# Kernel tuning notes

Measured on AMD Instinct MI355X. Metric: run time of the kernel, lower is better.

The kernel has to match this reference:

```python
import jax, jax.numpy as jnp
import numpy as np


def setup_inputs() -> dict:
    key = jax.random.key(0)
    ks = jax.random.split(key, 10)
    B, L, H, E, D = 2, 2048, 16, 64, 64
    d_model = 512
    inp = {
        "queries": jax.random.normal(ks[0], (B, L, H, E), jnp.float32),
        "keys": jax.random.normal(ks[1], (B, L, H, E), jnp.float32),
        "values": jax.random.normal(ks[2], (B, L, H, D), jnp.float32),
        "raw_series": jax.random.normal(ks[3], (B, L, d_model), jnp.float32),
        # learned fusion MLP: Linear(d_model, d_model//2) -> ReLU -> Linear(d_model//2, 1)
        "w1": jax.random.normal(ks[4], (d_model, d_model // 2), jnp.float32) / np.sqrt(d_model),
        "b1": jnp.zeros((d_model // 2,), jnp.float32),
        "w2": jax.random.normal(ks[5], (d_model // 2, 1), jnp.float32) / np.sqrt(d_model // 2),
        "b2": jnp.zeros((1,), jnp.float32),
        # per-head trend scaling, init ones
        "alpha_trend": jnp.ones((H,), jnp.float32),
    }
    return inp


MOMENTUM_ALPHA = 1.0
MOMENTUM_K = 1


def reference(queries, keys, values, raw_series, w1, b1, w2, b2, alpha_trend):
    B, L, H, E = queries.shape
    scale = 1.0 / jnp.sqrt(jnp.asarray(E, queries.dtype))

    # ---- soft momentum bias ----
    # learned fusion: MLP over features -> scalar per position, [B, L]
    h = jax.nn.relu(raw_series @ w1 + b1)
    fused = (h @ w2 + b2)[..., 0]                       # [B, L]
    k = max(1, min(MOMENTUM_K, L - 1))
    momentum = fused[:, k:] - fused[:, :-k]              # [B, L-k]
    momentum = jnp.pad(momentum, ((0, 0), (k, 0)))       # left-pad zeros -> [B, L]
    diff = jnp.abs(momentum[:, :, None] - momentum[:, None, :])  # [B, L, L]
    soft_bias = -MOMENTUM_ALPHA * diff                   # [B, L, L]

    # ---- attention ----
    scores = jnp.einsum('blhe,bshe->bhls', queries, keys)  # [B, H, L, L]
    scores = scores + soft_bias[:, None, :, :] * alpha_trend[None, :, None, None]
    causal = jnp.triu(jnp.ones((L, L), bool), k=1)       # True above diagonal
    scores = jnp.where(causal[None, None], -jnp.inf, scores)
    A = jax.nn.softmax(scale * scores, axis=-1)          # [B, H, L, L]
    V = jnp.einsum('bhls,bshd->blhd', A, values)         # [B, L, H, D]
    return V
```

## Files before the change

### kernel.cpp

```cpp
#include <hip/hip_runtime.h>
#include <math.h>

#define B_ 2
#define L_ 2048
#define H_ 16
#define E_ 64
#define D_ 64
#define DM_ 512
#define DH_ 256

typedef __bf16 bf16_t;
typedef bf16_t bf16x8_t __attribute__((ext_vector_type(8)));
typedef float f32x4_t __attribute__((ext_vector_type(4)));

__device__ __forceinline__ unsigned bpack(float hi, float lo) {
    unsigned uh = __float_as_uint(hi) + 0x8000u;
    unsigned ul = __float_as_uint(lo) + 0x8000u;
    return __builtin_amdgcn_perm(uh, ul, 0x07060302u);
}

__device__ __forceinline__ bf16_t to_bf16(float f) {
    union { float f; unsigned u; } x; x.f = f;
    unsigned r = (x.u + 0x7fffu + ((x.u >> 16) & 1u)) >> 16;
    union { unsigned short s; bf16_t b; } y; y.s = (unsigned short)r;
    return y.b;
}

__device__ __forceinline__ void gload_lds16(const bf16_t* g, bf16_t* l) {
    __builtin_amdgcn_global_load_lds(
        (const __attribute__((address_space(1))) unsigned int*)g,
        (__attribute__((address_space(3))) unsigned int*)l, 16, 0, 0);
}

__device__ __forceinline__ int permK(int sl) {
    return (sl & 3) | (((sl >> 3) & 1) << 2) | (((sl >> 4) & 1) << 3)
         | (((sl >> 2) & 1) << 4) | (((sl >> 5) & 1) << 5);
}

__global__ __launch_bounds__(256) void prep_kernel(
        const float* __restrict__ w1, bf16_t* __restrict__ w1t,
        const float* __restrict__ K, bf16_t* __restrict__ Kp,
        const float* __restrict__ V, bf16_t* __restrict__ Vs) {
    __shared__ bf16_t T[64][88];
    const int bidx = blockIdx.x;
    const int t = threadIdx.x;

    if (bidx < 256) {
        const int n = bidx;
        #pragma unroll
        for (int u = 0; u < 2; ++u) {
            int k = t + u * 256;
            w1t[(size_t)n * DM_ + k] = to_bf16(w1[(size_t)k * DH_ + n]);
        }
        return;
    }

    if (bidx < 1280) {
        const int idx = bidx - 256;
        const int bh = idx >> 5, tile = idx & 31;
        const int b = bh >> 4, h = bh & 15;
        const int sl = t >> 2, e0 = (t & 3) << 4;
        const float* src = K + (((size_t)b * L_ + tile * 64 + sl) * H_ + h) * E_ + e0;
        f32x4_t v0 = *(const f32x4_t*)(src);
        f32x4_t v1 = *(const f32x4_t*)(src + 4);
        f32x4_t v2 = *(const f32x4_t*)(src + 8);
        f32x4_t v3 = *(const f32x4_t*)(src + 12);
        uint4 lo, hi;
        lo.x = bpack(v0[1], v0[0]); lo.y = bpack(v0[3], v0[2]);
        lo.z = bpack(v1[1], v1[0]); lo.w = bpack(v1[3], v1[2]);
        hi.x = bpack(v2[1], v2[0]); hi.y = bpack(v2[3], v2[2]);
        hi.z = bpack(v3[1], v3[0]); hi.w = bpack(v3[3], v3[2]);
        const int r = permK(sl);
        const int bb = r & 7;
        bf16_t* drow = Kp + ((size_t)(bh * 32 + tile) * 64 + r) * 64;
        *(uint4*)(drow + ((((e0 >> 3)    ) ^ bb) << 3)) = lo;
        *(uint4*)(drow + ((((e0 >> 3) + 1) ^ bb) << 3)) = hi;
        return;
    }

    {
        const int idx = bidx - 1280;
        const int bh = idx >> 5, tile = idx & 31;
        const int b = bh >> 4, h = bh & 15;
        const int sl = t >> 2, d0 = (t & 3) << 4;
        const float* src = V + (((size_t)b * L_ + tile * 64 + sl) * H_ + h) * D_ + d0;
        f32x4_t v0 = *(const f32x4_t*)(src);
        f32x4_t v1 = *(const f32x4_t*)(src + 4);
        f32x4_t v2 = *(const f32x4_t*)(src + 8);
        f32x4_t v3 = *(const f32x4_t*)(src + 12);
        uint4 lo, hi;
        lo.x = bpack(v0[1], v0[0]); lo.y = bpack(v0[3], v0[2]);
        lo.z = bpack(v1[1], v1[0]); lo.w = bpack(v1[3], v1[2]);
        hi.x = bpack(v2[1], v2[0]); hi.y = bpack(v2[3], v2[2]);
        hi.z = bpack(v3[1], v3[0]); hi.w = bpack(v3[3], v3[2]);
        *(uint4*)&T[sl][d0]     = lo;
        *(uint4*)&T[sl][d0 + 8] = hi;
        __syncthreads();
        const int d = t & 63, bd = d & 7;
        bf16_t* drow = Vs + ((size_t)bh * 64 + d) * 2048 + tile * 64;
        #pragma unroll
        for (int gg = 0; gg < 2; ++gg) {
            int qb = (t >> 6) + gg * 4;
            int slb = (qb ^ bd) << 3;
            union { unsigned short u[8]; uint4 q; } acc;
            #pragma unroll
            for (int j = 0; j < 8; ++j) {
                union { bf16_t b; unsigned short s; } x; x.b = T[slb + j][d];
                acc.u[j] = x.s;
            }
            *(uint4*)(drow + qb * 8) = acc.q;
        }
    }
}

__global__ __launch_bounds__(256) void mlp_kernel(
        const float* __restrict__ raw, const bf16_t* __restrict__ w1t,
        const float* __restrict__ b1, const float* __restrict__ w2,
        const float* __restrict__ b2, float* __restrict__ fused) {
    __shared__ bf16_t Rs[16][520];
    __shared__ float part[4][16];
    const int t = threadIdx.x;
    const int m0 = blockIdx.x * 16;
    #pragma unroll
    for (int u = 0; u < 8; ++u) {
        int idx = t + u * 256;
        int row = idx >> 7;
        int k = (idx & 127) << 2;
        f32x4_t v = *(const f32x4_t*)&raw[(size_t)(m0 + row) * DM_ + k];
        uint2 p;
        p.x = bpack(v[1], v[0]);
        p.y = bpack(v[3], v[2]);
        *(uint2*)&Rs[row][k] = p;
    }
    __syncthreads();
    const int wave = t >> 6;
    const int lane = t & 63;
    const int lrow = lane & 15;
    const int lgrp = lane >> 4;
    const int n0w = wave * 64;

    f32x4_t acc[4];
    #pragma unroll
    for (int nt = 0; nt < 4; ++nt) acc[nt] = (f32x4_t){0.f, 0.f, 0.f, 0.f};

    const bf16_t* wbase = w1t + (size_t)(n0w + lrow) * DM_ + lgrp * 8;
    #pragma unroll
    for (int s = 0; s < 16; ++s) {
        bf16x8_t a = *(const bf16x8_t*)&Rs[lrow][s * 32 + lgrp * 8];
        #pragma unroll
        for (int nt = 0; nt < 4; ++nt) {
            bf16x8_t b = *(const bf16x8_t*)(wbase + nt * 16 * DM_ + s * 32);
            acc[nt] = __builtin_amdgcn_mfma_f32_16x16x32_bf16(a, b, acc[nt], 0, 0, 0);
        }
    }
    float rowpart[4] = {0.f, 0.f, 0.f, 0.f};
    #pragma unroll
    for (int nt = 0; nt < 4; ++nt) {
        int n = n0w + nt * 16 + lrow;
        float b1v = b1[n];
        float w2v = w2[n];
        #pragma unroll
        for (int r = 0; r < 4; ++r) {
            float h = acc[nt][r] + b1v;
            h = h > 0.f ? h : 0.f;
            rowpart[r] += h * w2v;
        }
    }
    #pragma unroll
    for (int r = 0; r < 4; ++r) {
        float v = rowpart[r];
        v += __shfl_xor(v, 1);
        v += __shfl_xor(v, 2);
        v += __shfl_xor(v, 4);
        v += __shfl_xor(v, 8);
        if (lrow == 0) part[wave][lgrp * 4 + r] = v;
    }
    __syncthreads();
    if (t < 16)
        fused[m0 + t] = part[0][t] + part[1][t] + part[2][t] + part[3][t] + b2[0];
}

__global__ __launch_bounds__(256) void attn_kernel(
        const float* __restrict__ Q, const bf16_t* __restrict__ Kp,
        const bf16_t* __restrict__ Vs, const float* __restrict__ fused,
        const float* __restrict__ alpha_trend, float* __restrict__ out) {
    __shared__ __align__(16) bf16_t Ks[2][64][64];
    __shared__ __align__(16) bf16_t Vt[2][64][64];
    __shared__ float moms[2][64];

    const int bid = blockIdx.x;
    const int bh  = bid & 31;
    const int grp = bid >> 5;
    const int qt  = (grp & 1) ? (grp >> 1) : 31 - (grp >> 1);
    const int h = bh & 15, b = bh >> 4;
    const int q0 = qt << 6;
    const int tid = threadIdx.x;
    const int wave = tid >> 6, lane = tid & 63;
    const int lrow = lane & 15, lgrp = lane >> 4;

    const float c1 = 0.18033688f;
    const float ascale2 = alpha_trend[h] * c1;
    const size_t bl = (size_t)b * L_;
    const int qw0 = q0 + wave * 16;

    const bf16_t* Kb = Kp + (size_t)bh * 131072;
    const bf16_t* Vb = Vs + (size_t)bh * 131072;
    const float* fusedp = fused + bl;

    bf16x8_t a_lo, a_hi;
    {
        const float* qp = Q + ((bl + qw0 + lrow) * H_ + h) * E_ + lgrp * 8;
        f32x4_t v0 = *(const f32x4_t*)(qp);
        f32x4_t v1 = *(const f32x4_t*)(qp + 4);
        f32x4_t v2 = *(const f32x4_t*)(qp + 32);
        f32x4_t v3 = *(const f32x4_t*)(qp + 36);
        #pragma unroll
        for (int k = 0; k < 4; ++k) {
            a_lo[k]     = to_bf16(v0[k] * c1);
            a_lo[4 + k] = to_bf16(v1[k] * c1);
            a_hi[k]     = to_bf16(v2[k] * c1);
            a_hi[4 + k] = to_bf16(v3[k] * c1);
        }
    }
    const int qg = qw0 + lrow;
    const float mq = (qg == 0) ? 0.f : fusedp[qg] - fusedp[qg - 1];

    const bf16_t* ksrc = Kb + wave * 512 + lane * 8;
    const bf16_t* vsrc = Vb + (size_t)(wave * 8 + (lane >> 3)) * 2048 + (lane & 7) * 8;

    f32x4_t Oacc[4];
    #pragma unroll
    for (int c = 0; c < 4; ++c) Oacc[c] = (f32x4_t){0.f, 0.f, 0.f, 0.f};
    float rowsum = 0.f;

    auto stage = [&](int t) {
        const int nb = t & 1;
        const bf16_t* kp0 = ksrc + (size_t)t * 4096;
        gload_lds16(kp0,        &Ks[nb][wave * 8][0]);
        gload_lds16(kp0 + 2048, &Ks[nb][wave * 8 + 32][0]);
        const bf16_t* vp0 = vsrc + t * 64;
        gload_lds16(vp0,               &Vt[nb][wave * 8][0]);
        gload_lds16(vp0 + 32 * 2048,   &Vt[nb][wave * 8 + 32][0]);
        if (tid < 64) {
            int s = t * 64 + tid;
            float f = fusedp[s];
            float fm = __shfl_up(f, 1);
            if (tid == 0) fm = (s == 0) ? f : fusedp[s - 1];
            moms[nb][tid] = f - fm;
        }
    };

    stage(0);
    for (int st = 0; st <= qt; ++st) {
        const int buf = st & 1;
        __syncthreads();
        if (st < qt) stage(st + 1);

        const char* ksb = (const char*)&Ks[buf][0][0];
        const char* vtb = (const char*)&Vt[buf][0][0];
        const int bb = lrow & 7;

        f32x4_t Sacc[4];
        #pragma unroll
        for (int c = 0; c < 4; ++c) Sacc[c] = (f32x4_t){0.f, 0.f, 0.f, 0.f};
        __builtin_amdgcn_s_setprio(1);
        #pragma unroll
        for (int c = 0; c < 4; ++c) {
            const char* kr = ksb + (c * 16 + lrow) * 128;
            bf16x8_t k_lo = *(const bf16x8_t*)(kr + ((lgrp ^ bb) << 4));
            bf16x8_t k_hi = *(const bf16x8_t*)(kr + (((4 + lgrp) ^ bb) << 4));
            Sacc[c] = __builtin_amdgcn_mfma_f32_16x16x32_bf16(k_lo, a_lo, Sacc[c], 0, 0, 0);
            Sacc[c] = __builtin_amdgcn_mfma_f32_16x16x32_bf16(k_hi, a_hi, Sacc[c], 0, 0, 0);
        }
        __builtin_amdgcn_s_setprio(0);

        float rowe[4][4];
        #pragma unroll
        for (int c = 0; c < 4; ++c) {
            const int sb = lgrp * 8 + ((c & 1) << 2) + ((c >> 1) << 5);
            f32x4_t ms4 = *(const f32x4_t*)&moms[buf][sb];
            #pragma unroll
            for (int r = 0; r < 4; ++r) {
                float arg = Sacc[c][r] - ascale2 * fabsf(mq - ms4[r]);
                rowe[c][r] = __builtin_amdgcn_exp2f(arg);
            }
        }
        if (st == qt) {
            const int s0 = st << 6;
            #pragma unroll
            for (int c = 0; c < 4; ++c) {
                const int sg0 = s0 + lgrp * 8 + ((c & 1) << 2) + ((c >> 1) << 5);
                #pragma unroll
                for (int r = 0; r < 4; ++r)
                    if (sg0 + r > qg) rowe[c][r] = 0.f;
            }
        }
        #pragma unroll
        for (int c = 0; c < 4; ++c)
            rowsum += (rowe[c][0] + rowe[c][1]) + (rowe[c][2] + rowe[c][3]);

        #pragma unroll
        for (int hh = 0; hh < 2; ++hh) {
            union { unsigned u[4]; bf16x8_t v; } pa;
            pa.u[0] = bpack(rowe[2 * hh][1],     rowe[2 * hh][0]);
            pa.u[1] = bpack(rowe[2 * hh][3],     rowe[2 * hh][2]);
            pa.u[2] = bpack(rowe[2 * hh + 1][1], rowe[2 * hh + 1][0]);
            pa.u[3] = bpack(rowe[2 * hh + 1][3], rowe[2 * hh + 1][2]);
            __builtin_amdgcn_s_setprio(1);
            #pragma unroll
            for (int c2 = 0; c2 < 4; ++c2) {
                const int row = c2 * 16 + lrow;
                bf16x8_t bv = *(const bf16x8_t*)(vtb + row * 128 +
                                                 (((hh * 4 + lgrp) ^ bb) << 4));
                Oacc[c2] = __builtin_amdgcn_mfma_f32_16x16x32_bf16(pa.v, bv, Oacc[c2], 0, 0, 0);
            }
            __builtin_amdgcn_s_setprio(0);
        }
    }

    float rs = rowsum;
    rs += __shfl_xor(rs, 16);
    rs += __shfl_xor(rs, 32);
    #pragma unroll
    for (int r = 0; r < 4; ++r) {
        float inv = 1.f / __shfl(rs, lgrp * 4 + r);
        size_t orow = ((bl + qw0 + lgrp * 4 + r) * H_ + h) * D_;
        #pragma unroll
        for (int c = 0; c < 4; ++c)
            out[orow + c * 16 + lrow] = Oacc[c][r] * inv;
    }
}

extern "C" void kernel_launch(void* const* d_in, const int* in_sizes, int n_in,
                              void* d_out, int out_size, void* d_ws, size_t ws_size,
                              hipStream_t stream) {
    const float* Q     = (const float*)d_in[0];
    const float* K     = (const float*)d_in[1];
    const float* V     = (const float*)d_in[2];
    const float* raw   = (const float*)d_in[3];
    const float* w1    = (const float*)d_in[4];
    const float* b1    = (const float*)d_in[5];
    const float* w2    = (const float*)d_in[6];
    const float* b2    = (const float*)d_in[7];
    const float* alpha = (const float*)d_in[8];
    float* out = (float*)d_out;

    float* fused = (float*)d_ws;
    bf16_t* w1t  = (bf16_t*)(fused + B_ * L_);
    bf16_t* Kp   = w1t + 256 * 512;
    bf16_t* Vs   = Kp + (size_t)B_ * H_ * L_ * E_;

    prep_kernel<<<2304, 256, 0, stream>>>(w1, w1t, K, Kp, V, Vs);
    mlp_kernel<<<B_ * L_ / 16, 256, 0, stream>>>(raw, w1t, b1, w2, b2, fused);
    attn_kernel<<<B_ * H_ * (L_ / 64), 256, 0, stream>>>(Q, Kp, Vs, fused, alpha, out);
}
```

Measured before the change: 169.5 us.

## Widen attention query tile to 128 rows and split MLP across N with atomics

The attention kernel now processes 128 query rows per block, with each wave handling two 16-row sub-tiles. Each staged K/V tile is reused for twice the queries, which halves K/V loads per query. Waves whose rows lie entirely before a key tile skip its compute, and blocks pair light and heavy tiles for causal balance. The MLP kernel is split four ways over hidden units, with partial sums combined by atomicAdd into a zeroed fused buffer and b2 dropped because momentum is a difference. The costs are more register pressure, half as many attention blocks, and idle waves on diagonal tiles.

```diff
diff --git a/kernel.cpp b/kernel.cpp
--- a/kernel.cpp
+++ b/kernel.cpp
@@ -40,7 +40,8 @@
 __global__ __launch_bounds__(256) void prep_kernel(
         const float* __restrict__ w1, bf16_t* __restrict__ w1t,
         const float* __restrict__ K, bf16_t* __restrict__ Kp,
-        const float* __restrict__ V, bf16_t* __restrict__ Vs) {
+        const float* __restrict__ V, bf16_t* __restrict__ Vs,
+        float* __restrict__ fused) {
     __shared__ bf16_t T[64][88];
     const int bidx = blockIdx.x;
     const int t = threadIdx.x;
@@ -51,6 +52,10 @@
         for (int u = 0; u < 2; ++u) {
             int k = t + u * 256;
             w1t[(size_t)n * DM_ + k] = to_bf16(w1[(size_t)k * DH_ + n]);
+        }
+        if (bidx == 0) {
+            #pragma unroll
+            for (int u = 0; u < 16; ++u) fused[t + u * 256] = 0.f;
         }
         return;
     }
@@ -116,11 +121,12 @@
 __global__ __launch_bounds__(256) void mlp_kernel(
         const float* __restrict__ raw, const bf16_t* __restrict__ w1t,
         const float* __restrict__ b1, const float* __restrict__ w2,
-        const float* __restrict__ b2, float* __restrict__ fused) {
+        float* __restrict__ fused) {
     __shared__ bf16_t Rs[16][520];
     __shared__ float part[4][16];
     const int t = threadIdx.x;
-    const int m0 = blockIdx.x * 16;
+    const int m0 = (blockIdx.x >> 2) * 16;
+    const int nq = blockIdx.x & 3;
     #pragma unroll
     for (int u = 0; u < 8; ++u) {
         int idx = t + u * 256;
@@ -137,34 +143,24 @@
     const int lane = t & 63;
     const int lrow = lane & 15;
     const int lgrp = lane >> 4;
-    const int n0w = wave * 64;
-
-    f32x4_t acc[4];
-    #pragma unroll
-    for (int nt = 0; nt < 4; ++nt) acc[nt] = (f32x4_t){0.f, 0.f, 0.f, 0.f};
-
-    const bf16_t* wbase = w1t + (size_t)(n0w + lrow) * DM_ + lgrp * 8;
+    const int n = nq * 64 + wave * 16 + lrow;
+
+    f32x4_t acc = (f32x4_t){0.f, 0.f, 0.f, 0.f};
+    const bf16_t* wbase = w1t + (size_t)n * DM_ + lgrp * 8;
     #pragma unroll
     for (int s = 0; s < 16; ++s) {
         bf16x8_t a = *(const bf16x8_t*)&Rs[lrow][s * 32 + lgrp * 8];
-        #pragma unroll
-        for (int nt = 0; nt < 4; ++nt) {
-            bf16x8_t b = *(const bf16x8_t*)(wbase + nt * 16 * DM_ + s * 32);
-            acc[nt] = __builtin_amdgcn_mfma_f32_16x16x32_bf16(a, b, acc[nt], 0, 0, 0);
-        }
-    }
-    float rowpart[4] = {0.f, 0.f, 0.f, 0.f};
-    #pragma unroll
-    for (int nt = 0; nt < 4; ++nt) {
-        int n = n0w + nt * 16 + lrow;
-        float b1v = b1[n];
-        float w2v = w2[n];
-        #pragma unroll
-        for (int r = 0; r < 4; ++r) {
-            float h = acc[nt][r] + b1v;
-            h = h > 0.f ? h : 0.f;
-            rowpart[r] += h * w2v;
-        }
+        bf16x8_t b = *(const bf16x8_t*)(wbase + s * 32);
+        acc = __builtin_amdgcn_mfma_f32_16x16x32_bf16(a, b, acc, 0, 0, 0);
+    }
+    const float b1v = b1[n];
+    const float w2v = w2[n];
+    float rowpart[4];
+    #pragma unroll
+    for (int r = 0; r < 4; ++r) {
+        float h = acc[r] + b1v;
+        h = h > 0.f ? h : 0.f;
+        rowpart[r] = h * w2v;
     }
     #pragma unroll
     for (int r = 0; r < 4; ++r) {
@@ -177,7 +173,7 @@
     }
     __syncthreads();
     if (t < 16)
-        fused[m0 + t] = part[0][t] + part[1][t] + part[2][t] + part[3][t] + b2[0];
+        atomicAdd(&fused[m0 + t], part[0][t] + part[1][t] + part[2][t] + part[3][t]);
 }
 
 __global__ __launch_bounds__(256) void attn_kernel(
@@ -191,9 +187,10 @@
     const int bid = blockIdx.x;
     const int bh  = bid & 31;
     const int grp = bid >> 5;
-    const int qt  = (grp & 1) ? (grp >> 1) : 31 - (grp >> 1);
+    const int tq  = (grp < 8) ? grp : 23 - grp;
     const int h = bh & 15, b = bh >> 4;
-    const int q0 = qt << 6;
+    const int q0 = tq << 7;
+    const int nsteps = 2 * tq + 2;
     const int tid = threadIdx.x;
     const int wave = tid >> 6, lane = tid & 63;
     const int lrow = lane & 15, lgrp = lane >> 4;
@@ -201,37 +198,51 @@
     const float c1 = 0.18033688f;
     const float ascale2 = alpha_trend[h] * c1;
     const size_t bl = (size_t)b * L_;
-    const int qw0 = q0 + wave * 16;
+    const int qw0 = q0 + wave * 32;
 
     const bf16_t* Kb = Kp + (size_t)bh * 131072;
     const bf16_t* Vb = Vs + (size_t)bh * 131072;
     const float* fusedp = fused + bl;
 
-    bf16x8_t a_lo, a_hi;
+    bf16x8_t a_lo, a_hi, c_lo, c_hi;
     {
         const float* qp = Q + ((bl + qw0 + lrow) * H_ + h) * E_ + lgrp * 8;
         f32x4_t v0 = *(const f32x4_t*)(qp);
         f32x4_t v1 = *(const f32x4_t*)(qp + 4);
         f32x4_t v2 = *(const f32x4_t*)(qp + 32);
         f32x4_t v3 = *(const f32x4_t*)(qp + 36);
+        const float* qp2 = qp + 16 * H_ * E_;
+        f32x4_t w0 = *(const f32x4_t*)(qp2);
+        f32x4_t w1v = *(const f32x4_t*)(qp2 + 4);
+        f32x4_t w2v = *(const f32x4_t*)(qp2 + 32);
+        f32x4_t w3 = *(const f32x4_t*)(qp2 + 36);
         #pragma unroll
         for (int k = 0; k < 4; ++k) {
             a_lo[k]     = to_bf16(v0[k] * c1);
             a_lo[4 + k] = to_bf16(v1[k] * c1);
             a_hi[k]     = to_bf16(v2[k] * c1);
             a_hi[4 + k] = to_bf16(v3[k] * c1);
-        }
-    }
-    const int qg = qw0 + lrow;
-    const float mq = (qg == 0) ? 0.f : fusedp[qg] - fusedp[qg - 1];
+            c_lo[k]     = to_bf16(w0[k] * c1);
+            c_lo[4 + k] = to_bf16(w1v[k] * c1);
+            c_hi[k]     = to_bf16(w2v[k] * c1);
+            c_hi[4 + k] = to_bf16(w3[k] * c1);
+        }
+    }
+    const int qg  = qw0 + lrow;
+    const int qg2 = qg + 16;
+    const float mq  = (qg == 0) ? 0.f : fusedp[qg] - fusedp[qg - 1];
+    const float mq2 = fusedp[qg2] - fusedp[qg2 - 1];
 
     const bf16_t* ksrc = Kb + wave * 512 + lane * 8;
     const bf16_t* vsrc = Vb + (size_t)(wave * 8 + (lane >> 3)) * 2048 + (lane & 7) * 8;
 
-    f32x4_t Oacc[4];
-    #pragma unroll
-    for (int c = 0; c < 4; ++c) Oacc[c] = (f32x4_t){0.f, 0.f, 0.f, 0.f};
-    float rowsum = 0.f;
+    f32x4_t Oacc[4], Oacc2[4];
+    #pragma unroll
+    for (int c = 0; c < 4; ++c) {
+        Oacc[c]  = (f32x4_t){0.f, 0.f, 0.f, 0.f};
+        Oacc2[c] = (f32x4_t){0.f, 0.f, 0.f, 0.f};
+    }
+    float rowsum = 0.f, rowsum2 = 0.f;
 
     auto stage = [&](int t) {
         const int nb = t & 1;
@@ -251,83 +262,105 @@
     };
 
     stage(0);
-    for (int st = 0; st <= qt; ++st) {
+    for (int st = 0; st < nsteps; ++st) {
         const int buf = st & 1;
         __syncthreads();
-        if (st < qt) stage(st + 1);
+        if (st + 1 < nsteps) stage(st + 1);
+
+        const int s0 = st << 6;
+        if (s0 > qw0) continue;
 
         const char* ksb = (const char*)&Ks[buf][0][0];
         const char* vtb = (const char*)&Vt[buf][0][0];
         const int bb = lrow & 7;
 
-        f32x4_t Sacc[4];
-        #pragma unroll
-        for (int c = 0; c < 4; ++c) Sacc[c] = (f32x4_t){0.f, 0.f, 0.f, 0.f};
+        f32x4_t Sacc[4], Sacc2[4];
+        #pragma unroll
+        for (int c = 0; c < 4; ++c) {
+            Sacc[c]  = (f32x4_t){0.f, 0.f, 0.f, 0.f};
+            Sacc2[c] = (f32x4_t){0.f, 0.f, 0.f, 0.f};
+        }
         __builtin_amdgcn_s_setprio(1);
         #pragma unroll
         for (int c = 0; c < 4; ++c) {
             const char* kr = ksb + (c * 16 + lrow) * 128;
             bf16x8_t k_lo = *(const bf16x8_t*)(kr + ((lgrp ^ bb) << 4));
             bf16x8_t k_hi = *(const bf16x8_t*)(kr + (((4 + lgrp) ^ bb) << 4));
-            Sacc[c] = __builtin_amdgcn_mfma_f32_16x16x32_bf16(k_lo, a_lo, Sacc[c], 0, 0, 0);
-            Sacc[c] = __builtin_amdgcn_mfma_f32_16x16x32_bf16(k_hi, a_hi, Sacc[c], 0, 0, 0);
+            Sacc[c]  = __builtin_amdgcn_mfma_f32_16x16x32_bf16(k_lo, a_lo, Sacc[c], 0, 0, 0);
+            Sacc2[c] = __builtin_amdgcn_mfma_f32_16x16x32_bf16(k_lo, c_lo, Sacc2[c], 0, 0, 0);
+            Sacc[c]  = __builtin_amdgcn_mfma_f32_16x16x32_bf16(k_hi, a_hi, Sacc[c], 0, 0, 0);
+            Sacc2[c] = __builtin_amdgcn_mfma_f32_16x16x32_bf16(k_hi, c_hi, Sacc2[c], 0, 0, 0);
         }
         __builtin_amdgcn_s_setprio(0);
 
-        float rowe[4][4];
+        float rowe[4][4], rowe2[4][4];
         #pragma unroll
         for (int c = 0; c < 4; ++c) {
             const int sb = lgrp * 8 + ((c & 1) << 2) + ((c >> 1) << 5);
             f32x4_t ms4 = *(const f32x4_t*)&moms[buf][sb];
             #pragma unroll
             for (int r = 0; r < 4; ++r) {
-                float arg = Sacc[c][r] - ascale2 * fabsf(mq - ms4[r]);
-                rowe[c][r] = __builtin_amdgcn_exp2f(arg);
+                float arg  = Sacc[c][r]  - ascale2 * fabsf(mq  - ms4[r]);
+                float arg2 = Sacc2[c][r] - ascale2 * fabsf(mq2 - ms4[r]);
+                rowe[c][r]  = __builtin_amdgcn_exp2f(arg);
+                rowe2[c][r] = __builtin_amdgcn_exp2f(arg2);
             }
         }
-        if (st == qt) {
-            const int s0 = st << 6;
+        if (qw0 - s0 < 64) {
             #pragma unroll
             for (int c = 0; c < 4; ++c) {
                 const int sg0 = s0 + lgrp * 8 + ((c & 1) << 2) + ((c >> 1) << 5);
                 #pragma unroll
-                for (int r = 0; r < 4; ++r)
-                    if (sg0 + r > qg) rowe[c][r] = 0.f;
+                for (int r = 0; r < 4; ++r) {
+                    if (sg0 + r > qg)  rowe[c][r]  = 0.f;
+                    if (sg0 + r > qg2) rowe2[c][r] = 0.f;
+                }
             }
         }
         #pragma unroll
-        for (int c = 0; c < 4; ++c)
-            rowsum += (rowe[c][0] + rowe[c][1]) + (rowe[c][2] + rowe[c][3]);
+        for (int c = 0; c < 4; ++c) {
+            rowsum  += (rowe[c][0]  + rowe[c][1])  + (rowe[c][2]  + rowe[c][3]);
+            rowsum2 += (rowe2[c][0] + rowe2[c][1]) + (rowe2[c][2] + rowe2[c][3]);
+        }
 
         #pragma unroll
         for (int hh = 0; hh < 2; ++hh) {
-            union { unsigned u[4]; bf16x8_t v; } pa;
-            pa.u[0] = bpack(rowe[2 * hh][1],     rowe[2 * hh][0]);
-            pa.u[1] = bpack(rowe[2 * hh][3],     rowe[2 * hh][2]);
-            pa.u[2] = bpack(rowe[2 * hh + 1][1], rowe[2 * hh + 1][0]);
-            pa.u[3] = bpack(rowe[2 * hh + 1][3], rowe[2 * hh + 1][2]);
+            union { unsigned u[4]; bf16x8_t v; } pa, pa2;
+            pa.u[0]  = bpack(rowe[2 * hh][1],      rowe[2 * hh][0]);
+            pa.u[1]  = bpack(rowe[2 * hh][3],      rowe[2 * hh][2]);
+            pa.u[2]  = bpack(rowe[2 * hh + 1][1],  rowe[2 * hh + 1][0]);
+            pa.u[3]  = bpack(rowe[2 * hh + 1][3],  rowe[2 * hh + 1][2]);
+            pa2.u[0] = bpack(rowe2[2 * hh][1],     rowe2[2 * hh][0]);
+            pa2.u[1] = bpack(rowe2[2 * hh][3],     rowe2[2 * hh][2]);
+            pa2.u[2] = bpack(rowe2[2 * hh + 1][1], rowe2[2 * hh + 1][0]);
+            pa2.u[3] = bpack(rowe2[2 * hh + 1][3], rowe2[2 * hh + 1][2]);
             __builtin_amdgcn_s_setprio(1);
             #pragma unroll
             for (int c2 = 0; c2 < 4; ++c2) {
                 const int row = c2 * 16 + lrow;
                 bf16x8_t bv = *(const bf16x8_t*)(vtb + row * 128 +
                                                  (((hh * 4 + lgrp) ^ bb) << 4));
-                Oacc[c2] = __builtin_amdgcn_mfma_f32_16x16x32_bf16(pa.v, bv, Oacc[c2], 0, 0, 0);
+                Oacc[c2]  = __builtin_amdgcn_mfma_f32_16x16x32_bf16(pa.v,  bv, Oacc[c2],  0, 0, 0);
+                Oacc2[c2] = __builtin_amdgcn_mfma_f32_16x16x32_bf16(pa2.v, bv, Oacc2[c2], 0, 0, 0);
             }
             __builtin_amdgcn_s_setprio(0);
         }
     }
 
-    float rs = rowsum;
-    rs += __shfl_xor(rs, 16);
-    rs += __shfl_xor(rs, 32);
+    float rs = rowsum, rs2 = rowsum2;
+    rs  += __shfl_xor(rs, 16);  rs  += __shfl_xor(rs, 32);
+    rs2 += __shfl_xor(rs2, 16); rs2 += __shfl_xor(rs2, 32);
     #pragma unroll
     for (int r = 0; r < 4; ++r) {
-        float inv = 1.f / __shfl(rs, lgrp * 4 + r);
-        size_t orow = ((bl + qw0 + lgrp * 4 + r) * H_ + h) * D_;
-        #pragma unroll
-        for (int c = 0; c < 4; ++c)
-            out[orow + c * 16 + lrow] = Oacc[c][r] * inv;
+        float inv  = 1.f / __shfl(rs,  lgrp * 4 + r);
+        float inv2 = 1.f / __shfl(rs2, lgrp * 4 + r);
+        size_t orow  = ((bl + qw0 + lgrp * 4 + r) * H_ + h) * D_;
+        size_t orow2 = orow + (size_t)16 * H_ * D_;
+        #pragma unroll
+        for (int c = 0; c < 4; ++c) {
+            out[orow  + c * 16 + lrow] = Oacc[c][r]  * inv;
+            out[orow2 + c * 16 + lrow] = Oacc2[c][r] * inv2;
+        }
     }
 }
 
@@ -341,7 +374,6 @@
     const float* w1    = (const float*)d_in[4];
     const float* b1    = (const float*)d_in[5];
     const float* w2    = (const float*)d_in[6];
-    const float* b2    = (const float*)d_in[7];
     const float* alpha = (const float*)d_in[8];
     float* out = (float*)d_out;
 
@@ -350,7 +382,7 @@
     bf16_t* Kp   = w1t + 256 * 512;
     bf16_t* Vs   = Kp + (size_t)B_ * H_ * L_ * E_;
 
-    prep_kernel<<<2304, 256, 0, stream>>>(w1, w1t, K, Kp, V, Vs);
-    mlp_kernel<<<B_ * L_ / 16, 256, 0, stream>>>(raw, w1t, b1, w2, b2, fused);
-    attn_kernel<<<B_ * H_ * (L_ / 64), 256, 0, stream>>>(Q, Kp, Vs, fused, alpha, out);
-}
+    prep_kernel<<<2304, 256, 0, stream>>>(w1, w1t, K, Kp, V, Vs, fused);
+    mlp_kernel<<<B_ * L_ / 16 * 4, 256, 0, stream>>>(raw, w1t, b1, w2, fused);
+    attn_kernel<<<B_ * H_ * (L_ / 128), 256, 0, stream>>>(Q, Kp, Vs, fused, alpha, out);
+}
```

Result: slower. 179.8 us (+6.1%).

## Process KV tiles in pairs, precompute momentum, split MLP hidden across blocks

Applied to the files above, without the earlier changes.

The attention kernel now stages two 64-key tiles per barrier, so there are half as many __syncthreads per query block. Each block also precomputes momentum for the whole sequence into shared memory once, instead of computing it per tile. The MLP kernel splits the hidden dimension across four blocks per row group and reduces with atomicAdd into a buffer zeroed in prep, which gives it more parallelism. The cost is more LDS per attention block, which may lower occupancy. Dropping b2 is valid because it cancels in the momentum difference, but atomics make the fused sum order non-deterministic.

```diff
diff --git a/kernel.cpp b/kernel.cpp
--- a/kernel.cpp
+++ b/kernel.cpp
@@ -40,7 +40,8 @@
 __global__ __launch_bounds__(256) void prep_kernel(
         const float* __restrict__ w1, bf16_t* __restrict__ w1t,
         const float* __restrict__ K, bf16_t* __restrict__ Kp,
-        const float* __restrict__ V, bf16_t* __restrict__ Vs) {
+        const float* __restrict__ V, bf16_t* __restrict__ Vs,
+        float* __restrict__ fused) {
     __shared__ bf16_t T[64][88];
     const int bidx = blockIdx.x;
     const int t = threadIdx.x;
@@ -51,6 +52,10 @@
         for (int u = 0; u < 2; ++u) {
             int k = t + u * 256;
             w1t[(size_t)n * DM_ + k] = to_bf16(w1[(size_t)k * DH_ + n]);
+        }
+        if (bidx == 0) {
+            #pragma unroll
+            for (int u = 0; u < 16; ++u) fused[t + u * 256] = 0.f;
         }
         return;
     }
@@ -116,11 +121,12 @@
 __global__ __launch_bounds__(256) void mlp_kernel(
         const float* __restrict__ raw, const bf16_t* __restrict__ w1t,
         const float* __restrict__ b1, const float* __restrict__ w2,
-        const float* __restrict__ b2, float* __restrict__ fused) {
+        float* __restrict__ fused) {
     __shared__ bf16_t Rs[16][520];
     __shared__ float part[4][16];
     const int t = threadIdx.x;
-    const int m0 = blockIdx.x * 16;
+    const int m0 = (blockIdx.x >> 2) * 16;
+    const int nq = blockIdx.x & 3;
     #pragma unroll
     for (int u = 0; u < 8; ++u) {
         int idx = t + u * 256;
@@ -137,34 +143,24 @@
     const int lane = t & 63;
     const int lrow = lane & 15;
     const int lgrp = lane >> 4;
-    const int n0w = wave * 64;
-
-    f32x4_t acc[4];
-    #pragma unroll
-    for (int nt = 0; nt < 4; ++nt) acc[nt] = (f32x4_t){0.f, 0.f, 0.f, 0.f};
-
-    const bf16_t* wbase = w1t + (size_t)(n0w + lrow) * DM_ + lgrp * 8;
+    const int n = nq * 64 + wave * 16 + lrow;
+
+    f32x4_t acc = (f32x4_t){0.f, 0.f, 0.f, 0.f};
+    const bf16_t* wbase = w1t + (size_t)n * DM_ + lgrp * 8;
     #pragma unroll
     for (int s = 0; s < 16; ++s) {
         bf16x8_t a = *(const bf16x8_t*)&Rs[lrow][s * 32 + lgrp * 8];
-        #pragma unroll
-        for (int nt = 0; nt < 4; ++nt) {
-            bf16x8_t b = *(const bf16x8_t*)(wbase + nt * 16 * DM_ + s * 32);
-            acc[nt] = __builtin_amdgcn_mfma_f32_16x16x32_bf16(a, b, acc[nt], 0, 0, 0);
-        }
-    }
-    float rowpart[4] = {0.f, 0.f, 0.f, 0.f};
-    #pragma unroll
-    for (int nt = 0; nt < 4; ++nt) {
-        int n = n0w + nt * 16 + lrow;
-        float b1v = b1[n];
-        float w2v = w2[n];
-        #pragma unroll
-        for (int r = 0; r < 4; ++r) {
-            float h = acc[nt][r] + b1v;
-            h = h > 0.f ? h : 0.f;
-            rowpart[r] += h * w2v;
-        }
+        bf16x8_t b = *(const bf16x8_t*)(wbase + s * 32);
+        acc = __builtin_amdgcn_mfma_f32_16x16x32_bf16(a, b, acc, 0, 0, 0);
+    }
+    const float b1v = b1[n];
+    const float w2v = w2[n];
+    float rowpart[4];
+    #pragma unroll
+    for (int r = 0; r < 4; ++r) {
+        float h = acc[r] + b1v;
+        h = h > 0.f ? h : 0.f;
+        rowpart[r] = h * w2v;
     }
     #pragma unroll
     for (int r = 0; r < 4; ++r) {
@@ -177,16 +173,16 @@
     }
     __syncthreads();
     if (t < 16)
-        fused[m0 + t] = part[0][t] + part[1][t] + part[2][t] + part[3][t] + b2[0];
+        atomicAdd(&fused[m0 + t], part[0][t] + part[1][t] + part[2][t] + part[3][t]);
 }
 
 __global__ __launch_bounds__(256) void attn_kernel(
         const float* __restrict__ Q, const bf16_t* __restrict__ Kp,
         const bf16_t* __restrict__ Vs, const float* __restrict__ fused,
         const float* __restrict__ alpha_trend, float* __restrict__ out) {
-    __shared__ __align__(16) bf16_t Ks[2][64][64];
-    __shared__ __align__(16) bf16_t Vt[2][64][64];
-    __shared__ float moms[2][64];
+    __shared__ __align__(16) bf16_t Ks[2][128][64];
+    __shared__ __align__(16) bf16_t Vt[2][128][64];
+    __shared__ __align__(16) float moms_all[2048];
 
     const int bid = blockIdx.x;
     const int bh  = bid & 31;
@@ -194,6 +190,7 @@
     const int qt  = (grp & 1) ? (grp >> 1) : 31 - (grp >> 1);
     const int h = bh & 15, b = bh >> 4;
     const int q0 = qt << 6;
+    const int npairs = (qt + 2) >> 1;
     const int tid = threadIdx.x;
     const int wave = tid >> 6, lane = tid & 63;
     const int lrow = lane & 15, lgrp = lane >> 4;
@@ -206,6 +203,14 @@
     const bf16_t* Kb = Kp + (size_t)bh * 131072;
     const bf16_t* Vb = Vs + (size_t)bh * 131072;
     const float* fusedp = fused + bl;
+
+    #pragma unroll
+    for (int u = 0; u < 8; ++u) {
+        int i = tid + u * 256;
+        float f = fusedp[i];
+        float fm = (i == 0) ? f : fusedp[i - 1];
+        moms_all[i] = f - fm;
+    }
 
     bf16x8_t a_lo, a_hi;
     {
@@ -233,88 +238,91 @@
     for (int c = 0; c < 4; ++c) Oacc[c] = (f32x4_t){0.f, 0.f, 0.f, 0.f};
     float rowsum = 0.f;
 
-    auto stage = [&](int t) {
-        const int nb = t & 1;
-        const bf16_t* kp0 = ksrc + (size_t)t * 4096;
+    auto stage = [&](int p) {
+        const int nb = p & 1;
+        const bf16_t* kp0 = ksrc + (size_t)p * 8192;
         gload_lds16(kp0,        &Ks[nb][wave * 8][0]);
         gload_lds16(kp0 + 2048, &Ks[nb][wave * 8 + 32][0]);
-        const bf16_t* vp0 = vsrc + t * 64;
-        gload_lds16(vp0,               &Vt[nb][wave * 8][0]);
-        gload_lds16(vp0 + 32 * 2048,   &Vt[nb][wave * 8 + 32][0]);
-        if (tid < 64) {
-            int s = t * 64 + tid;
-            float f = fusedp[s];
-            float fm = __shfl_up(f, 1);
-            if (tid == 0) fm = (s == 0) ? f : fusedp[s - 1];
-            moms[nb][tid] = f - fm;
-        }
+        gload_lds16(kp0 + 4096, &Ks[nb][64 + wave * 8][0]);
+        gload_lds16(kp0 + 6144, &Ks[nb][64 + wave * 8 + 32][0]);
+        const bf16_t* vp0 = vsrc + p * 128;
+        gload_lds16(vp0,                  &Vt[nb][wave * 8][0]);
+        gload_lds16(vp0 + 32 * 2048,      &Vt[nb][wave * 8 + 32][0]);
+        gload_lds16(vp0 + 64,             &Vt[nb][64 + wave * 8][0]);
+        gload_lds16(vp0 + 64 + 32 * 2048, &Vt[nb][64 + wave * 8 + 32][0]);
     };
 
     stage(0);
-    for (int st = 0; st <= qt; ++st) {
-        const int buf = st & 1;
+    for (int p = 0; p < npairs; ++p) {
         __syncthreads();
-        if (st < qt) stage(st + 1);
-
-        const char* ksb = (const char*)&Ks[buf][0][0];
-        const char* vtb = (const char*)&Vt[buf][0][0];
+        if (p + 1 < npairs) stage(p + 1);
+        const int nb = p & 1;
         const int bb = lrow & 7;
 
-        f32x4_t Sacc[4];
-        #pragma unroll
-        for (int c = 0; c < 4; ++c) Sacc[c] = (f32x4_t){0.f, 0.f, 0.f, 0.f};
-        __builtin_amdgcn_s_setprio(1);
-        #pragma unroll
-        for (int c = 0; c < 4; ++c) {
-            const char* kr = ksb + (c * 16 + lrow) * 128;
-            bf16x8_t k_lo = *(const bf16x8_t*)(kr + ((lgrp ^ bb) << 4));
-            bf16x8_t k_hi = *(const bf16x8_t*)(kr + (((4 + lgrp) ^ bb) << 4));
-            Sacc[c] = __builtin_amdgcn_mfma_f32_16x16x32_bf16(k_lo, a_lo, Sacc[c], 0, 0, 0);
-            Sacc[c] = __builtin_amdgcn_mfma_f32_16x16x32_bf16(k_hi, a_hi, Sacc[c], 0, 0, 0);
-        }
-        __builtin_amdgcn_s_setprio(0);
-
-        float rowe[4][4];
-        #pragma unroll
-        for (int c = 0; c < 4; ++c) {
-            const int sb = lgrp * 8 + ((c & 1) << 2) + ((c >> 1) << 5);
-            f32x4_t ms4 = *(const f32x4_t*)&moms[buf][sb];
-            #pragma unroll
-            for (int r = 0; r < 4; ++r) {
-                float arg = Sacc[c][r] - ascale2 * fabsf(mq - ms4[r]);
-                rowe[c][r] = __builtin_amdgcn_exp2f(arg);
-            }
-        }
-        if (st == qt) {
-            const int s0 = st << 6;
+        #pragma unroll
+        for (int sub = 0; sub < 2; ++sub) {
+            const int tile = 2 * p + sub;
+            const int s0 = tile << 6;
+            if (s0 > qw0) continue;
+
+            const char* ksb = (const char*)&Ks[nb][sub * 64][0];
+            const char* vtb = (const char*)&Vt[nb][sub * 64][0];
+
+            f32x4_t Sacc[4];
+            #pragma unroll
+            for (int c = 0; c < 4; ++c) Sacc[c] = (f32x4_t){0.f, 0.f, 0.f, 0.f};
+            __builtin_amdgcn_s_setprio(1);
             #pragma unroll
             for (int c = 0; c < 4; ++c) {
-                const int sg0 = s0 + lgrp * 8 + ((c & 1) << 2) + ((c >> 1) << 5);
+                const char* kr = ksb + (c * 16 + lrow) * 128;
+                bf16x8_t k_lo = *(const bf16x8_t*)(kr + ((lgrp ^ bb) << 4));
+                bf16x8_t k_hi = *(const bf16x8_t*)(kr + (((4 + lgrp) ^ bb) << 4));
+                Sacc[c] = __builtin_amdgcn_mfma_f32_16x16x32_bf16(k_lo, a_lo, Sacc[c], 0, 0, 0);
+                Sacc[c] = __builtin_amdgcn_mfma_f32_16x16x32_bf16(k_hi, a_hi, Sacc[c], 0, 0, 0);
+            }
+            __builtin_amdgcn_s_setprio(0);
+
+            float rowe[4][4];
+            #pragma unroll
+            for (int c = 0; c < 4; ++c) {
+                const int sb = lgrp * 8 + ((c & 1) << 2) + ((c >> 1) << 5);
+                f32x4_t ms4 = *(const f32x4_t*)&moms_all[s0 + sb];
                 #pragma unroll
-                for (int r = 0; r < 4; ++r)
-                    if (sg0 + r > qg) rowe[c][r] = 0.f;
-            }
-        }
-        #pragma unroll
-        for (int c = 0; c < 4; ++c)
-            rowsum += (rowe[c][0] + rowe[c][1]) + (rowe[c][2] + rowe[c][3]);
-
-        #pragma unroll
-        for (int hh = 0; hh < 2; ++hh) {
-            union { unsigned u[4]; bf16x8_t v; } pa;
-            pa.u[0] = bpack(rowe[2 * hh][1],     rowe[2 * hh][0]);
-            pa.u[1] = bpack(rowe[2 * hh][3],     rowe[2 * hh][2]);
-            pa.u[2] = bpack(rowe[2 * hh + 1][1], rowe[2 * hh + 1][0]);
-            pa.u[3] = bpack(rowe[2 * hh + 1][3], rowe[2 * hh + 1][2]);
-            __builtin_amdgcn_s_setprio(1);
-            #pragma unroll
-            for (int c2 = 0; c2 < 4; ++c2) {
-                const int row = c2 * 16 + lrow;
-                bf16x8_t bv = *(const bf16x8_t*)(vtb + row * 128 +
-                                                 (((hh * 4 + lgrp) ^ bb) << 4));
-                Oacc[c2] = __builtin_amdgcn_mfma_f32_16x16x32_bf16(pa.v, bv, Oacc[c2], 0, 0, 0);
-            }
-            __builtin_amdgcn_s_setprio(0);
+                for (int r = 0; r < 4; ++r) {
+                    float arg = Sacc[c][r] - ascale2 * fabsf(mq - ms4[r]);
+                    rowe[c][r] = __builtin_amdgcn_exp2f(arg);
+                }
+            }
+            if (tile == qt) {
+                #pragma unroll
+                for (int c = 0; c < 4; ++c) {
+                    const int sg0 = s0 + lgrp * 8 + ((c & 1) << 2) + ((c >> 1) << 5);
+                    #pragma unroll
+                    for (int r = 0; r < 4; ++r)
+                        if (sg0 + r > qg) rowe[c][r] = 0.f;
+                }
+            }
+            #pragma unroll
+            for (int c = 0; c < 4; ++c)
+                rowsum += (rowe[c][0] + rowe[c][1]) + (rowe[c][2] + rowe[c][3]);
+
+            #pragma unroll
+            for (int hh = 0; hh < 2; ++hh) {
+                union { unsigned u[4]; bf16x8_t v; } pa;
+                pa.u[0] = bpack(rowe[2 * hh][1],     rowe[2 * hh][0]);
+                pa.u[1] = bpack(rowe[2 * hh][3],     rowe[2 * hh][2]);
+                pa.u[2] = bpack(rowe[2 * hh + 1][1], rowe[2 * hh + 1][0]);
+                pa.u[3] = bpack(rowe[2 * hh + 1][3], rowe[2 * hh + 1][2]);
+                __builtin_amdgcn_s_setprio(1);
+                #pragma unroll
+                for (int c2 = 0; c2 < 4; ++c2) {
+                    const int row = c2 * 16 + lrow;
+                    bf16x8_t bv = *(const bf16x8_t*)(vtb + row * 128 +
+                                                     (((hh * 4 + lgrp) ^ bb) << 4));
+                    Oacc[c2] = __builtin_amdgcn_mfma_f32_16x16x32_bf16(pa.v, bv, Oacc[c2], 0, 0, 0);
+                }
+                __builtin_amdgcn_s_setprio(0);
+            }
         }
     }
 
@@ -341,7 +349,6 @@
     const float* w1    = (const float*)d_in[4];
     const float* b1    = (const float*)d_in[5];
     const float* w2    = (const float*)d_in[6];
-    const float* b2    = (const float*)d_in[7];
     const float* alpha = (const float*)d_in[8];
     float* out = (float*)d_out;
 
@@ -350,7 +357,7 @@
     bf16_t* Kp   = w1t + 256 * 512;
     bf16_t* Vs   = Kp + (size_t)B_ * H_ * L_ * E_;
 
-    prep_kernel<<<2304, 256, 0, stream>>>(w1, w1t, K, Kp, V, Vs);
-    mlp_kernel<<<B_ * L_ / 16, 256, 0, stream>>>(raw, w1t, b1, w2, b2, fused);
+    prep_kernel<<<2304, 256, 0, stream>>>(w1, w1t, K, Kp, V, Vs, fused);
+    mlp_kernel<<<B_ * L_ / 16 * 4, 256, 0, stream>>>(raw, w1t, b1, w2, fused);
     attn_kernel<<<B_ * H_ * (L_ / 64), 256, 0, stream>>>(Q, Kp, Vs, fused, alpha, out);
 }
```

After: 169.6 us. About the same (+0.0%).
